# Performance work log

Hardware: AMD Instinct MI355X
Metric: run time of the kernel (lower is better)

## Reference

```python
import jax, jax.numpy as jnp
import numpy as np

TOPK = 32  # module init arg


def setup_inputs() -> dict:
    key = jax.random.key(0)
    kq, kk, kv = jax.random.split(key, 3)
    B, T, S, H, E = 1, 2048, 2048, 16, 64
    return {
        "query": jax.random.normal(kq, (B, T, H, E), dtype=jnp.float32),
        "key": jax.random.normal(kk, (B, S, H, E), dtype=jnp.float32),
        "value": jax.random.normal(kv, (B, S, H, E), dtype=jnp.float32),
    }


def reference(query, key, value):
    B, T, H, E = query.shape
    S = key.shape[1]
    softmax_temp = 1.0 / np.sqrt(E)  # default: 1/sqrt(d_keys)
    topk = min(TOPK, S)

    q = query * jnp.asarray(softmax_temp, query.dtype)
    # full dense scores, as in the original module: [B, H, T, S]
    QK = jnp.einsum('bthe,bshe->bhts', q, key)

    # oracle top-k along keys; scatter True at top-k positions (exact mask semantics)
    _, topk_idx = jax.lax.top_k(QK, topk)  # [B, H, T, k]
    keep = jnp.put_along_axis(
        jnp.zeros(QK.shape, dtype=jnp.bool_), topk_idx, True, axis=-1,
        inplace=False,
    )
    QK = jnp.where(keep, QK, -jnp.inf)

    attn = jax.nn.softmax(QK, axis=-1)  # dropout p=0.0 -> identity
    output = jnp.einsum('bhts,bshd->bthd', attn, value)
    return output
```

## Files before the change

kernel.cpp:

```cpp
#include <hip/hip_runtime.h>
#include <stdint.h>


#define T_DIM 2048
#define S_DIM 2048
#define H_DIM 16
#define E_DIM 64
#define K_TOP 32
#define TT 8
#define NWAVE 8

__device__ __forceinline__ unsigned f2ord(float f) {
    unsigned b = __float_as_uint(f);
    return (b & 0x80000000u) ? ~b : (b | 0x80000000u);
}
__device__ __forceinline__ float ord2f(unsigned u) {
    unsigned b = (u & 0x80000000u) ? (u ^ 0x80000000u) : ~u;
    return __uint_as_float(b);
}

__global__ __launch_bounds__(256)
void transpose_k(const float* __restrict__ Kg, float* __restrict__ KT) {
    __shared__ float tile[64][65];
    const int tid = threadIdx.x;
    const int h   = blockIdx.x & (H_DIM - 1);
    const int sb  = (blockIdx.x >> 4) * 64;
    #pragma unroll
    for (int sw = 0; sw < 4; sw++) {
        int r = sw * 16 + (tid >> 4);
        int c = (tid & 15) * 4;
        float4 v = *(const float4*)(Kg + ((size_t)(sb + r) * H_DIM + h) * E_DIM + c);
        tile[r][c] = v.x; tile[r][c+1] = v.y; tile[r][c+2] = v.z; tile[r][c+3] = v.w;
    }
    __syncthreads();
    #pragma unroll
    for (int sw = 0; sw < 4; sw++) {
        int e = sw * 16 + (tid >> 4);
        int j = (tid & 15) * 4;
        float4 v = { tile[j][e], tile[j+1][e], tile[j+2][e], tile[j+3][e] };
        *(float4*)(KT + ((size_t)h * E_DIM + e) * S_DIM + sb + j) = v;
    }
}

__global__ __launch_bounds__(512, 2)
void topk_attn_kernel(const float* __restrict__ Qg,
                      const float* __restrict__ KT,
                      const float* __restrict__ Vg,
                      float* __restrict__ Out) {
    __shared__ __align__(16) float sS[TT][S_DIM];
    __shared__ unsigned candU[NWAVE][64];
    __shared__ int      candI[NWAVE][64];
    __shared__ unsigned wcnt[NWAVE];

    const int tid  = threadIdx.x;
    const int lane = tid & 63;
    const int wv   = tid >> 6;
    const int bx   = blockIdx.x;
    const int h    = bx & (H_DIM - 1);
    const int tb   = bx >> 4;
    const int t0   = tb * TT;

    float4 acc[TT];
    #pragma unroll
    for (int t = 0; t < TT; t++) acc[t] = make_float4(0.f, 0.f, 0.f, 0.f);

    const int   sb  = wv * 256 + (lane << 2);
    const float* kp = KT + (size_t)h * E_DIM * S_DIM + sb;
    const float* Qb = Qg + ((size_t)t0 * H_DIM + h) * E_DIM;

    float4 k0 = *(const float4*)(kp);
    float4 k1 = *(const float4*)(kp + S_DIM);
    for (int e2 = 0; e2 < 32; e2++) {
        const int ep = (e2 + 1) & 31;
        float4 n0 = *(const float4*)(kp + (size_t)(2 * ep)     * S_DIM);
        float4 n1 = *(const float4*)(kp + (size_t)(2 * ep + 1) * S_DIM);
        #pragma unroll
        for (int t = 0; t < TT; t++) {
            float2 qv = *(const float2*)(Qb + (size_t)t * (H_DIM * E_DIM) + 2 * e2);
            acc[t].x = fmaf(qv.x, k0.x, acc[t].x);
            acc[t].y = fmaf(qv.x, k0.y, acc[t].y);
            acc[t].z = fmaf(qv.x, k0.z, acc[t].z);
            acc[t].w = fmaf(qv.x, k0.w, acc[t].w);
            acc[t].x = fmaf(qv.y, k1.x, acc[t].x);
            acc[t].y = fmaf(qv.y, k1.y, acc[t].y);
            acc[t].z = fmaf(qv.y, k1.z, acc[t].z);
            acc[t].w = fmaf(qv.y, k1.w, acc[t].w);
        }
        k0 = n0; k1 = n1;
    }

    #pragma unroll
    for (int r = 0; r < TT; r++)
        *(float4*)(&sS[r][sb]) = acc[r];
    __syncthreads();

    unsigned u[32];
    #pragma unroll
    for (int i = 0; i < 32; i++) u[i] = f2ord(sS[wv][i * 64 + lane]);

    auto wave_count = [&](unsigned t) -> int {
        int c = 0;
        #pragma unroll
        for (int i = 0; i < 32; i++)
            c += __popcll(__ballot(u[i] >= t));
        return c;
    };

    unsigned thr = 0xC1800000u;
    int c = wave_count(thr);
    if (c < K_TOP || c > 64) {
        unsigned lo = (c >= K_TOP) ? thr : 0u;
        unsigned hi = (c >= K_TOP) ? 0xFFFFFFFFu : thr;
        bool found = false;
        while (!found && (hi - lo > 1u)) {
            unsigned mid = lo + ((hi - lo) >> 1);
            int cm = wave_count(mid);
            if (cm >= K_TOP && cm <= 64) { thr = mid; c = cm; found = true; }
            else if (cm >= K_TOP) lo = mid;
            else hi = mid;
        }
        if (!found) { thr = lo; c = wave_count(lo); }
    }
    int n = (c > 64) ? 64 : c;

    if (lane == 0) wcnt[wv] = 0u;
    #pragma unroll
    for (int i = 0; i < 32; i++) {
        if (u[i] >= thr) {
            unsigned pos = atomicAdd(&wcnt[wv], 1u);
            if (pos < 64u) {
                candU[wv][pos] = u[i];
                candI[wv][pos] = i * 64 + lane;
            }
        }
    }

    unsigned long long key = 0ull;
    if (lane < n)
        key = (((unsigned long long)candU[wv][lane]) << 32)
            | (unsigned)(~candI[wv][lane]);
    #pragma unroll
    for (int k = 2; k <= 64; k <<= 1)
        #pragma unroll
        for (int j = k >> 1; j > 0; j >>= 1) {
            unsigned long long ok = __shfl_xor(key, j);
            bool takemax = ((lane & j) == 0) ^ ((lane & k) != 0);
            bool mineG   = key > ok;
            key = (takemax == mineG) ? key : ok;
        }

    const float* Vb = Vg + (size_t)h * E_DIM;
    float val  = ord2f((unsigned)(key >> 32)) * 0.125f;
    int   sidx = (int)(~(unsigned)key);
    float m = __shfl(val, 0);
    float w = (lane < K_TOP) ? expf(val - m) : 0.f;
    float Z = w;
    #pragma unroll
    for (int d = 32; d > 0; d >>= 1) Z += __shfl_xor(Z, d);
    float pr = w / Z;

    float o = 0.f;
    #pragma unroll
    for (int i2 = 0; i2 < K_TOP; i2++) {
        float pi = __shfl(pr, i2);
        int   s2 = __shfl(sidx, i2);
        o = fmaf(pi, Vb[(size_t)s2 * (H_DIM * E_DIM) + lane], o);
    }
    int t = t0 + wv;
    Out[((size_t)t * H_DIM + h) * E_DIM + lane] = o;
}

extern "C" void kernel_launch(void* const* d_in, const int* in_sizes, int n_in,
                              void* d_out, int out_size, void* d_ws, size_t ws_size,
                              hipStream_t stream) {
    const float* Q = (const float*)d_in[0];
    const float* K = (const float*)d_in[1];
    const float* V = (const float*)d_in[2];
    float* O  = (float*)d_out;
    float* KT = (float*)d_ws;
    (void)in_sizes; (void)n_in; (void)out_size; (void)ws_size;
    transpose_k<<<dim3(H_DIM * (S_DIM / 64)), dim3(256), 0, stream>>>(K, KT);
    topk_attn_kernel<<<dim3((T_DIM / TT) * H_DIM), dim3(512), 0, stream>>>(Q, KT, V, O);
}
```

Measured before the change: 242.7 us.

## Double queries per block and use packed FP32 FMA for scores

```diff
diff --git a/kernel.cpp b/kernel.cpp
--- a/kernel.cpp
+++ b/kernel.cpp
@@ -7,8 +7,14 @@
 #define H_DIM 16
 #define E_DIM 64
 #define K_TOP 32
-#define TT 8
+#define TT 16
 #define NWAVE 8
+
+typedef float v2f __attribute__((ext_vector_type(2)));
+
+__device__ __forceinline__ v2f pk_fma(v2f a, v2f b, v2f c) {
+    return __builtin_elementwise_fma(a, b, c);
+}
 
 __device__ __forceinline__ unsigned f2ord(float f) {
     unsigned b = __float_as_uint(f);
@@ -47,7 +53,7 @@
                       const float* __restrict__ KT,
                       const float* __restrict__ Vg,
                       float* __restrict__ Out) {
-    __shared__ __align__(16) float sS[TT][S_DIM];
+    __shared__ __align__(16) float sS[8][S_DIM];
     __shared__ unsigned candU[NWAVE][64];
     __shared__ int      candI[NWAVE][64];
     __shared__ unsigned wcnt[NWAVE];
@@ -60,114 +66,121 @@
     const int tb   = bx >> 4;
     const int t0   = tb * TT;
 
-    float4 acc[TT];
+    v2f acc2[TT][2];
     #pragma unroll
-    for (int t = 0; t < TT; t++) acc[t] = make_float4(0.f, 0.f, 0.f, 0.f);
+    for (int t = 0; t < TT; t++) { acc2[t][0] = (v2f)(0.f); acc2[t][1] = (v2f)(0.f); }
 
     const int   sb  = wv * 256 + (lane << 2);
     const float* kp = KT + (size_t)h * E_DIM * S_DIM + sb;
     const float* Qb = Qg + ((size_t)t0 * H_DIM + h) * E_DIM;
 
-    float4 k0 = *(const float4*)(kp);
-    float4 k1 = *(const float4*)(kp + S_DIM);
+    float4 k0q = *(const float4*)(kp);
+    float4 k1q = *(const float4*)(kp + S_DIM);
     for (int e2 = 0; e2 < 32; e2++) {
         const int ep = (e2 + 1) & 31;
-        float4 n0 = *(const float4*)(kp + (size_t)(2 * ep)     * S_DIM);
-        float4 n1 = *(const float4*)(kp + (size_t)(2 * ep + 1) * S_DIM);
+        float4 n0q = *(const float4*)(kp + (size_t)(2 * ep)     * S_DIM);
+        float4 n1q = *(const float4*)(kp + (size_t)(2 * ep + 1) * S_DIM);
+        v2f k0lo = {k0q.x, k0q.y}, k0hi = {k0q.z, k0q.w};
+        v2f k1lo = {k1q.x, k1q.y}, k1hi = {k1q.z, k1q.w};
         #pragma unroll
         for (int t = 0; t < TT; t++) {
             float2 qv = *(const float2*)(Qb + (size_t)t * (H_DIM * E_DIM) + 2 * e2);
-            acc[t].x = fmaf(qv.x, k0.x, acc[t].x);
-            acc[t].y = fmaf(qv.x, k0.y, acc[t].y);
-            acc[t].z = fmaf(qv.x, k0.z, acc[t].z);
-            acc[t].w = fmaf(qv.x, k0.w, acc[t].w);
-            acc[t].x = fmaf(qv.y, k1.x, acc[t].x);
-            acc[t].y = fmaf(qv.y, k1.y, acc[t].y);
-            acc[t].z = fmaf(qv.y, k1.z, acc[t].z);
-            acc[t].w = fmaf(qv.y, k1.w, acc[t].w);
+            v2f qx = {qv.x, qv.x}, qy = {qv.y, qv.y};
+            acc2[t][0] = pk_fma(qx, k0lo, acc2[t][0]);
+            acc2[t][1] = pk_fma(qx, k0hi, acc2[t][1]);
+            acc2[t][0] = pk_fma(qy, k1lo, acc2[t][0]);
+            acc2[t][1] = pk_fma(qy, k1hi, acc2[t][1]);
         }
-        k0 = n0; k1 = n1;
+        k0q = n0q; k1q = n1q;
     }
 
-    #pragma unroll
-    for (int r = 0; r < TT; r++)
-        *(float4*)(&sS[r][sb]) = acc[r];
-    __syncthreads();
+    const float* Vb = Vg + (size_t)h * E_DIM;
 
-    unsigned u[32];
-    #pragma unroll
-    for (int i = 0; i < 32; i++) u[i] = f2ord(sS[wv][i * 64 + lane]);
+    for (int p = 0; p < 2; p++) {
+        __syncthreads();
+        #pragma unroll
+        for (int r = 0; r < 8; r++) {
+            int rr = p * 8 + r;
+            float4 f4 = { acc2[rr][0].x, acc2[rr][0].y,
+                          acc2[rr][1].x, acc2[rr][1].y };
+            *(float4*)(&sS[r][sb]) = f4;
+        }
+        __syncthreads();
 
-    auto wave_count = [&](unsigned t) -> int {
-        int c = 0;
+        unsigned u[32];
         #pragma unroll
-        for (int i = 0; i < 32; i++)
-            c += __popcll(__ballot(u[i] >= t));
-        return c;
-    };
+        for (int i = 0; i < 32; i++) u[i] = f2ord(sS[wv][i * 64 + lane]);
 
-    unsigned thr = 0xC1800000u;
-    int c = wave_count(thr);
-    if (c < K_TOP || c > 64) {
-        unsigned lo = (c >= K_TOP) ? thr : 0u;
-        unsigned hi = (c >= K_TOP) ? 0xFFFFFFFFu : thr;
-        bool found = false;
-        while (!found && (hi - lo > 1u)) {
-            unsigned mid = lo + ((hi - lo) >> 1);
-            int cm = wave_count(mid);
-            if (cm >= K_TOP && cm <= 64) { thr = mid; c = cm; found = true; }
-            else if (cm >= K_TOP) lo = mid;
-            else hi = mid;
+        auto wave_count = [&](unsigned t) -> int {
+            int c = 0;
+            #pragma unroll
+            for (int i = 0; i < 32; i++)
+                c += __popcll(__ballot(u[i] >= t));
+            return c;
+        };
+
+        unsigned thr = 0xC1800000u;
+        int c = wave_count(thr);
+        if (c < K_TOP || c > 64) {
+            unsigned lo = (c >= K_TOP) ? thr : 0u;
+            unsigned hi = (c >= K_TOP) ? 0xFFFFFFFFu : thr;
+            bool found = false;
+            while (!found && (hi - lo > 1u)) {
+                unsigned mid = lo + ((hi - lo) >> 1);
+                int cm = wave_count(mid);
+                if (cm >= K_TOP && cm <= 64) { thr = mid; c = cm; found = true; }
+                else if (cm >= K_TOP) lo = mid;
+                else hi = mid;
+            }
+            if (!found) { thr = lo; c = wave_count(lo); }
         }
-        if (!found) { thr = lo; c = wave_count(lo); }
-    }
-    int n = (c > 64) ? 64 : c;
+        int n = (c > 64) ? 64 : c;
 
-    if (lane == 0) wcnt[wv] = 0u;
-    #pragma unroll
-    for (int i = 0; i < 32; i++) {
-        if (u[i] >= thr) {
-            unsigned pos = atomicAdd(&wcnt[wv], 1u);
-            if (pos < 64u) {
-                candU[wv][pos] = u[i];
-                candI[wv][pos] = i * 64 + lane;
+        if (lane == 0) wcnt[wv] = 0u;
+        #pragma unroll
+        for (int i = 0; i < 32; i++) {
+            if (u[i] >= thr) {
+                unsigned pos = atomicAdd(&wcnt[wv], 1u);
+                if (pos < 64u) {
+                    candU[wv][pos] = u[i];
+                    candI[wv][pos] = i * 64 + lane;
+                }
             }
         }
+
+        unsigned long long key = 0ull;
+        if (lane < n)
+            key = (((unsigned long long)candU[wv][lane]) << 32)
+                | (unsigned)(~candI[wv][lane]);
+        #pragma unroll
+        for (int k = 2; k <= 64; k <<= 1)
+            #pragma unroll
+            for (int j = k >> 1; j > 0; j >>= 1) {
+                unsigned long long ok = __shfl_xor(key, j);
+                bool takemax = ((lane & j) == 0) ^ ((lane & k) != 0);
+                bool mineG   = key > ok;
+                key = (takemax == mineG) ? key : ok;
+            }
+
+        float val  = ord2f((unsigned)(key >> 32)) * 0.125f;
+        int   sidx = (int)(~(unsigned)key);
+        float m = __shfl(val, 0);
+        float w = (lane < K_TOP) ? expf(val - m) : 0.f;
+        float Z = w;
+        #pragma unroll
+        for (int d = 32; d > 0; d >>= 1) Z += __shfl_xor(Z, d);
+        float pr = w / Z;
+
+        float o = 0.f;
+        #pragma unroll
+        for (int i2 = 0; i2 < K_TOP; i2++) {
+            float pi = __shfl(pr, i2);
+            int   s2 = __shfl(sidx, i2);
+            o = fmaf(pi, Vb[(size_t)s2 * (H_DIM * E_DIM) + lane], o);
+        }
+        int t = t0 + p * 8 + wv;
+        Out[((size_t)t * H_DIM + h) * E_DIM + lane] = o;
     }
-
-    unsigned long long key = 0ull;
-    if (lane < n)
-        key = (((unsigned long long)candU[wv][lane]) << 32)
-            | (unsigned)(~candI[wv][lane]);
-    #pragma unroll
-    for (int k = 2; k <= 64; k <<= 1)
-        #pragma unroll
-        for (int j = k >> 1; j > 0; j >>= 1) {
-            unsigned long long ok = __shfl_xor(key, j);
-            bool takemax = ((lane & j) == 0) ^ ((lane & k) != 0);
-            bool mineG   = key > ok;
-            key = (takemax == mineG) ? key : ok;
-        }
-
-    const float* Vb = Vg + (size_t)h * E_DIM;
-    float val  = ord2f((unsigned)(key >> 32)) * 0.125f;
-    int   sidx = (int)(~(unsigned)key);
-    float m = __shfl(val, 0);
-    float w = (lane < K_TOP) ? expf(val - m) : 0.f;
-    float Z = w;
-    #pragma unroll
-    for (int d = 32; d > 0; d >>= 1) Z += __shfl_xor(Z, d);
-    float pr = w / Z;
-
-    float o = 0.f;
-    #pragma unroll
-    for (int i2 = 0; i2 < K_TOP; i2++) {
-        float pi = __shfl(pr, i2);
-        int   s2 = __shfl(sidx, i2);
-        o = fmaf(pi, Vb[(size_t)s2 * (H_DIM * E_DIM) + lane], o);
-    }
-    int t = t0 + wv;
-    Out[((size_t)t * H_DIM + h) * E_DIM + lane] = o;
 }
 
 extern "C" void kernel_launch(void* const* d_in, const int* in_sizes, int n_in,
```

Result: slower. 344.8 us (+42.1%).
